# Performance work log

Measured on AMD Instinct MI355X. Metric: run time of the kernel, lower is better.

The kernel has to match this reference:

```python
import jax, jax.numpy as jnp
import numpy as np

N_NODES = 50000
N_EDGES = 1600000
NODE_DIM = 64
EDGE_DIM = 64
HID = 64
EPS = 1e-5


def _linear(x, W, b):
    return x @ W + b


def _layernorm(x, g, b):
    m = jnp.mean(x, axis=-1, keepdims=True)
    v = jnp.mean((x - m) ** 2, axis=-1, keepdims=True)
    return (x - m) * jax.lax.rsqrt(v + EPS) * g + b


def _mlp(x, p, pre):
    # Linear-ReLU, Linear-ReLU, Linear-LayerNorm
    h = jax.nn.relu(_linear(x, p[pre + 'W1'], p[pre + 'b1']))
    h = jax.nn.relu(_linear(h, p[pre + 'W2'], p[pre + 'b2']))
    h = _linear(h, p[pre + 'W3'], p[pre + 'b3'])
    return _layernorm(h, p[pre + 'g'], p[pre + 'beta'])


def setup_inputs() -> dict:
    key = jax.random.key(0)
    ks = jax.random.split(key, 16)
    inp = {
        'node_feat': jax.random.normal(ks[0], (N_NODES, NODE_DIM), jnp.float32),
        'edge_feat': jax.random.normal(ks[1], (N_EDGES, EDGE_DIM), jnp.float32),
        'edge_idx': jax.random.randint(ks[2], (N_EDGES, 2), 0, N_NODES, jnp.int32),
        'node_size': N_NODES,
    }
    s = 0.05
    e_in = EDGE_DIM + 2 * NODE_DIM
    n_in = NODE_DIM + EDGE_DIM
    inp['eW1'] = jax.random.normal(ks[3], (e_in, HID), jnp.float32) * s
    inp['eb1'] = jnp.zeros((HID,), jnp.float32)
    inp['eW2'] = jax.random.normal(ks[4], (HID, HID), jnp.float32) * s
    inp['eb2'] = jnp.zeros((HID,), jnp.float32)
    inp['eW3'] = jax.random.normal(ks[5], (HID, HID), jnp.float32) * s
    inp['eb3'] = jnp.zeros((HID,), jnp.float32)
    inp['eg'] = jnp.ones((HID,), jnp.float32)
    inp['ebeta'] = jnp.zeros((HID,), jnp.float32)
    inp['nW1'] = jax.random.normal(ks[6], (n_in, HID), jnp.float32) * s
    inp['nb1'] = jnp.zeros((HID,), jnp.float32)
    inp['nW2'] = jax.random.normal(ks[7], (HID, HID), jnp.float32) * s
    inp['nb2'] = jnp.zeros((HID,), jnp.float32)
    inp['nW3'] = jax.random.normal(ks[8], (HID, HID), jnp.float32) * s
    inp['nb3'] = jnp.zeros((HID,), jnp.float32)
    inp['ng'] = jnp.ones((HID,), jnp.float32)
    inp['nbeta'] = jnp.zeros((HID,), jnp.float32)
    return inp


def reference(node_feat, edge_feat, edge_idx, node_size,
              eW1, eb1, eW2, eb2, eW3, eb3, eg, ebeta,
              nW1, nb1, nW2, nb2, nW3, nb3, ng, nbeta):
    p = dict(eW1=eW1, eb1=eb1, eW2=eW2, eb2=eb2, eW3=eW3, eb3=eb3, eg=eg, ebeta=ebeta,
             nW1=nW1, nb1=nb1, nW2=nW2, nb2=nb2, nW3=nW3, nb3=nb3, ng=ng, nbeta=nbeta)
    center = edge_idx[:, 0]
    source = edge_idx[:, 1]
    # [E, edge_dim + 2*node_dim]
    stacked = jnp.concatenate([edge_feat, node_feat[center], node_feat[source]], axis=1)
    proc_edge_feat = _mlp(stacked, p, 'e')  # [E, 64]
    # scatter-add aggregate to nodes
    nodal_edge_feat = jax.ops.segment_sum(proc_edge_feat, center, num_segments=node_size)
    stacked_node = jnp.concatenate([node_feat, nodal_edge_feat], axis=1)  # [N, node_dim+64]
    proc_node_feat = _mlp(stacked_node, p, 'n')  # [N, 64]
    return proc_edge_feat, proc_node_feat
```

## Files before the change

kernel.cpp:

```cpp
#include <hip/hip_runtime.h>

typedef unsigned short u16;
typedef unsigned int u32;
typedef __attribute__((ext_vector_type(8))) __bf16 bf16x8;
typedef __attribute__((ext_vector_type(4))) float f32x4;
typedef __attribute__((ext_vector_type(2))) u32 u32x2;
typedef __attribute__((ext_vector_type(4))) u32 u32x4;

__device__ __forceinline__ u16 f2bf(float f) {
    u32 u = __float_as_uint(f);
    u = (u + 0x7FFFu + ((u >> 16) & 1u)) >> 16;
    return (u16)u;
}
__device__ __forceinline__ bf16x8 cvt2bf(f32x4 lo, f32x4 hi) {
    bf16x8 r;
    r[0] = (__bf16)lo[0]; r[1] = (__bf16)lo[1]; r[2] = (__bf16)lo[2]; r[3] = (__bf16)lo[3];
    r[4] = (__bf16)hi[0]; r[5] = (__bf16)hi[1]; r[6] = (__bf16)hi[2]; r[7] = (__bf16)hi[3];
    return r;
}
__device__ __forceinline__ bf16x8 load8f_bf(const float* p) {
    return cvt2bf(*(const f32x4*)p, *(const f32x4*)(p + 4));
}
__device__ __forceinline__ u32 pk2(float x, float y) {
    __bf16 bx = (__bf16)x, by = (__bf16)y;
    return (u32)__builtin_bit_cast(u16, bx) | ((u32)__builtin_bit_cast(u16, by) << 16);
}

#define PK_EW1 0
#define PK_EW2 12288
#define PK_EW3 16384
#define PK_NW1 20480
#define PK_NW2 28672
#define PK_NW3 32768
#define PK_TOTAL 36864

__global__ void pack_weights_kernel(const float* __restrict__ eW1, const float* __restrict__ eW2,
                                    const float* __restrict__ eW3, const float* __restrict__ nW1,
                                    const float* __restrict__ nW2, const float* __restrict__ nW3,
                                    u16* __restrict__ P) {
    int idx = blockIdx.x * blockDim.x + threadIdx.x;
    if (idx >= PK_TOTAL) return;
    const float* W; int base;
    if (idx < PK_EW2)      { W = eW1; base = PK_EW1; }
    else if (idx < PK_EW3) { W = eW2; base = PK_EW2; }
    else if (idx < PK_NW1) { W = eW3; base = PK_EW3; }
    else if (idx < PK_NW2) { W = nW1; base = PK_NW1; }
    else if (idx < PK_NW3) { W = nW2; base = PK_NW2; }
    else                   { W = nW3; base = PK_NW3; }
    int r = idx - base;
    int j = r & 7, lane = (r >> 3) & 63, m = (r >> 9) & 3, s = r >> 11;
    int k = s * 32 + (lane >> 4) * 8 + j;
    int col = 16 * m + (lane & 15);
    P[idx] = f2bf(W[k * 64 + col]);
}

__global__ void degree_kernel(const int* __restrict__ edge_idx, int* __restrict__ deg, int E) {
    int e = blockIdx.x * blockDim.x + threadIdx.x;
    if (e < E) atomicAdd(&deg[edge_idx[2 * e]], 1);
}

__global__ void scan_blocks_kernel(const int* __restrict__ deg, int* __restrict__ off,
                                   int* __restrict__ partials, int N) {
    __shared__ int sh[256];
    const int t = threadIdx.x;
    const int g = blockIdx.x * 256 + t;
    int v = (g < N) ? deg[g] : 0;
    sh[t] = v;
    __syncthreads();
#pragma unroll
    for (int d = 1; d < 256; d <<= 1) {
        int add = (t >= d) ? sh[t - d] : 0;
        __syncthreads();
        sh[t] += add;
        __syncthreads();
    }
    if (g < N) off[g] = sh[t] - v;
    if (t == 255) partials[blockIdx.x] = sh[255];
}

__global__ void scan_partials_kernel(int* __restrict__ partials, int nparts) {
    __shared__ int sh[256];
    const int t = threadIdx.x;
    int v = (t < nparts) ? partials[t] : 0;
    sh[t] = v;
    __syncthreads();
#pragma unroll
    for (int d = 1; d < 256; d <<= 1) {
        int add = (t >= d) ? sh[t - d] : 0;
        __syncthreads();
        sh[t] += add;
        __syncthreads();
    }
    if (t < nparts) partials[t] = sh[t] - v;
}

__global__ void finalize_offsets_kernel(int* __restrict__ off, int* __restrict__ pos,
                                        const int* __restrict__ partials, int N, int E) {
    int g = blockIdx.x * blockDim.x + threadIdx.x;
    if (g < N) {
        int o = off[g] + partials[g >> 8];
        off[g] = o;
        pos[g] = o;
    }
    if (g == 0) off[N] = E;
}

__global__ void fill_csr_kernel(const int* __restrict__ edge_idx, int* __restrict__ pos,
                                int* __restrict__ csr, int E) {
    int e = blockIdx.x * blockDim.x + threadIdx.x;
    if (e < E) {
        int slot = atomicAdd(&pos[edge_idx[2 * e]], 1);
        csr[slot] = e;
    }
}

__global__ __launch_bounds__(256) void gather_csr_kernel(
    const float* __restrict__ proc_edge, const int* __restrict__ off,
    const int* __restrict__ csr, u16* __restrict__ nodal16, int N)
{
    const int wid = threadIdx.x >> 6, lane = threadIdx.x & 63;
    const int n = blockIdx.x * 4 + wid;
    if (n >= N) return;
    const int r = lane >> 4;
    const int q = lane & 15;
    const int beg = off[n], end = off[n + 1];
    f32x4 v0 = 0.0f, v1 = 0.0f, v2 = 0.0f, v3 = 0.0f;
    int j = beg + r;
    for (; j + 12 < end; j += 16) {
        int e0 = csr[j], e1 = csr[j + 4], e2 = csr[j + 8], e3 = csr[j + 12];
        v0 += *(const f32x4*)(proc_edge + (size_t)e0 * 64 + q * 4);
        v1 += *(const f32x4*)(proc_edge + (size_t)e1 * 64 + q * 4);
        v2 += *(const f32x4*)(proc_edge + (size_t)e2 * 64 + q * 4);
        v3 += *(const f32x4*)(proc_edge + (size_t)e3 * 64 + q * 4);
    }
    for (; j < end; j += 4) {
        int e0 = csr[j];
        v0 += *(const f32x4*)(proc_edge + (size_t)e0 * 64 + q * 4);
    }
    v0 += v1; v2 += v3; v0 += v2;
#pragma unroll
    for (int i = 0; i < 4; ++i) {
        v0[i] += __shfl_xor(v0[i], 16, 64);
        v0[i] += __shfl_xor(v0[i], 32, 64);
    }
    if (r == 0) {
        u32x2 pv; pv[0] = pk2(v0[0], v0[1]); pv[1] = pk2(v0[2], v0[3]);
        *(u32x2*)(nodal16 + (size_t)n * 64 + q * 4) = pv;
    }
}

__global__ __launch_bounds__(256) void edge_mlp_kernel(
    const float* __restrict__ node_feat, const float* __restrict__ edge_feat,
    const int* __restrict__ edge_idx, const u16* __restrict__ Pw,
    const float* __restrict__ b1g, const float* __restrict__ b2g, const float* __restrict__ b3g,
    const float* __restrict__ gg, const float* __restrict__ betag,
    float* __restrict__ out_edge, int E)
{
    __shared__ u16 wlds[12288];
    __shared__ u16 stage[4][6144];
    __shared__ float params[5][64];
    const int tid = threadIdx.x;
#pragma unroll
    for (int i = 0; i < 6; ++i) {
        int idx = i * 256 + tid;
        *(u32x4*)(wlds + (size_t)idx * 8) = *(const u32x4*)(Pw + PK_EW1 + (size_t)idx * 8);
    }
    if (tid < 64) {
        params[0][tid] = b1g[tid];
        params[1][tid] = b2g[tid];
        params[2][tid] = b3g[tid];
        params[3][tid] = gg[tid];
        params[4][tid] = betag[tid];
    }
    __syncthreads();

    const int wid = tid >> 6, lane = tid & 63;
    const int er = lane & 15, a = lane >> 4;
    const int e0 = blockIdx.x * 64 + wid * 16 + er;
    const int e = (e0 < E) ? e0 : (E - 1);
    int2 ii = *(const int2*)(edge_idx + 2 * e);
    const int cn = ii.x, sn = ii.y;
    u16* st = stage[wid];
    const int swz = (er & 7) << 4;

#pragma unroll
    for (int s = 0; s < 6; ++s) {
        const float* base;
        if (s < 2)      base = edge_feat + (size_t)e * 64 + s * 32 + a * 8;
        else if (s < 4) base = node_feat + (size_t)cn * 64 + (s - 2) * 32 + a * 8;
        else            base = node_feat + (size_t)sn * 64 + (s - 4) * 32 + a * 8;
        __builtin_amdgcn_global_load_lds(
            (const __attribute__((address_space(1))) void*)base,
            (__attribute__((address_space(3))) void*)(st + (2 * s) * 512), 16, 0, 0);
        __builtin_amdgcn_global_load_lds(
            (const __attribute__((address_space(1))) void*)(base + 4),
            (__attribute__((address_space(3))) void*)(st + (2 * s + 1) * 512), 16, 0, 0);
    }
    __builtin_amdgcn_sched_barrier(0);
    asm volatile("s_waitcnt vmcnt(0)" ::: "memory");
    __builtin_amdgcn_sched_barrier(0);

    f32x4 acc[4];
#pragma unroll
    for (int m = 0; m < 4; ++m) acc[m] = 0.0f;
#pragma unroll
    for (int s = 0; s < 6; ++s) {
        f32x4 lo = *(const f32x4*)((const char*)st + (2 * s) * 1024 + lane * 16);
        f32x4 hi = *(const f32x4*)((const char*)st + (2 * s + 1) * 1024 + lane * 16);
        bf16x8 bf = cvt2bf(lo, hi);
#pragma unroll
        for (int m = 0; m < 4; ++m) {
            bf16x8 af = *(const bf16x8*)(wlds + ((s * 4 + m) * 64 + lane) * 8);
            acc[m] = __builtin_amdgcn_mfma_f32_16x16x32_bf16(af, bf, acc[m], 0, 0, 0);
        }
    }
    __syncthreads();
#pragma unroll
    for (int i = 0; i < 4; ++i) {
        int idx = i * 256 + tid;
        *(u32x4*)(wlds + (size_t)idx * 8) = *(const u32x4*)(Pw + PK_EW2 + (size_t)idx * 8);
    }
    __syncthreads();

    u16* ht = st;
#pragma unroll
    for (int m = 0; m < 4; ++m) {
        float v0 = fmaxf(acc[m][0] + params[0][16 * m + 4 * a + 0], 0.0f);
        float v1 = fmaxf(acc[m][1] + params[0][16 * m + 4 * a + 1], 0.0f);
        float v2 = fmaxf(acc[m][2] + params[0][16 * m + 4 * a + 2], 0.0f);
        float v3 = fmaxf(acc[m][3] + params[0][16 * m + 4 * a + 3], 0.0f);
        u32x2 pv; pv[0] = pk2(v0, v1); pv[1] = pk2(v2, v3);
        int boff = (er * 128 + (16 * m + 4 * a) * 2) ^ swz;
        *(u32x2*)((char*)ht + boff) = pv;
    }
    f32x4 a2[4];
#pragma unroll
    for (int m = 0; m < 4; ++m) a2[m] = 0.0f;
#pragma unroll
    for (int s = 0; s < 2; ++s) {
        int boff = (er * 128 + s * 64 + a * 16) ^ swz;
        bf16x8 bf = *(const bf16x8*)((char*)ht + boff);
#pragma unroll
        for (int m = 0; m < 4; ++m) {
            bf16x8 af = *(const bf16x8*)(wlds + ((s * 4 + m) * 64 + lane) * 8);
            a2[m] = __builtin_amdgcn_mfma_f32_16x16x32_bf16(af, bf, a2[m], 0, 0, 0);
        }
    }
#pragma unroll
    for (int m = 0; m < 4; ++m) {
        float v0 = fmaxf(a2[m][0] + params[1][16 * m + 4 * a + 0], 0.0f);
        float v1 = fmaxf(a2[m][1] + params[1][16 * m + 4 * a + 1], 0.0f);
        float v2 = fmaxf(a2[m][2] + params[1][16 * m + 4 * a + 2], 0.0f);
        float v3 = fmaxf(a2[m][3] + params[1][16 * m + 4 * a + 3], 0.0f);
        u32x2 pv; pv[0] = pk2(v0, v1); pv[1] = pk2(v2, v3);
        int boff = (er * 128 + (16 * m + 4 * a) * 2) ^ swz;
        *(u32x2*)((char*)ht + boff) = pv;
    }
    f32x4 a3[4];
#pragma unroll
    for (int m = 0; m < 4; ++m) a3[m] = 0.0f;
#pragma unroll
    for (int s = 0; s < 2; ++s) {
        int boff = (er * 128 + s * 64 + a * 16) ^ swz;
        bf16x8 bf = *(const bf16x8*)((char*)ht + boff);
#pragma unroll
        for (int m = 0; m < 4; ++m) {
            bf16x8 af = *(const bf16x8*)(wlds + 4096 + ((s * 4 + m) * 64 + lane) * 8);
            a3[m] = __builtin_amdgcn_mfma_f32_16x16x32_bf16(af, bf, a3[m], 0, 0, 0);
        }
    }
    float vals[16], sum = 0.0f, ssq = 0.0f;
#pragma unroll
    for (int m = 0; m < 4; ++m)
#pragma unroll
        for (int r = 0; r < 4; ++r) {
            float v = a3[m][r] + params[2][16 * m + 4 * a + r];
            vals[4 * m + r] = v; sum += v; ssq += v * v;
        }
    sum += __shfl_xor(sum, 16, 64); sum += __shfl_xor(sum, 32, 64);
    ssq += __shfl_xor(ssq, 16, 64); ssq += __shfl_xor(ssq, 32, 64);
    const float mean = sum * 0.015625f;
    const float var = ssq * 0.015625f - mean * mean;
    const float inv = rsqrtf(var + 1e-5f);
    if (e0 < E) {
#pragma unroll
        for (int m = 0; m < 4; ++m) {
            f32x4 o;
#pragma unroll
            for (int r = 0; r < 4; ++r) {
                int f = 16 * m + 4 * a + r;
                o[r] = (vals[4 * m + r] - mean) * inv * params[3][f] + params[4][f];
            }
            *(f32x4*)(out_edge + (size_t)e0 * 64 + 16 * m + 4 * a) = o;
        }
    }
}

__global__ __launch_bounds__(256) void node_mlp_kernel(
    const float* __restrict__ node_feat, const u16* __restrict__ nodal16,
    const u16* __restrict__ Pw,
    const float* __restrict__ b1g, const float* __restrict__ b2g, const float* __restrict__ b3g,
    const float* __restrict__ gg, const float* __restrict__ betag,
    float* __restrict__ out_node, int N)
{
    __shared__ float params[5][64];
    __shared__ u16 htile[4][1024];
    const int tid = threadIdx.x;
    if (tid < 64) {
        params[0][tid] = b1g[tid];
        params[1][tid] = b2g[tid];
        params[2][tid] = b3g[tid];
        params[3][tid] = gg[tid];
        params[4][tid] = betag[tid];
    }
    __syncthreads();
    const int wid = tid >> 6, lane = tid & 63;
    const int er = lane & 15, a = lane >> 4;
    const int nbase = (blockIdx.x * 4 + wid) * 16;
    if (nbase >= N) return;
    const int n = nbase + er;
    u16* ht = htile[wid];
    const int swz = (er & 7) << 4;

    f32x4 acc[4];
#pragma unroll
    for (int m = 0; m < 4; ++m) acc[m] = 0.0f;

#pragma unroll
    for (int s = 0; s < 4; ++s) {
        bf16x8 af[4];
#pragma unroll
        for (int m = 0; m < 4; ++m)
            af[m] = *(const bf16x8*)(Pw + PK_NW1 + ((s * 4 + m) * 64 + lane) * 8);
        bf16x8 bf;
        if (s < 2) bf = load8f_bf(node_feat + (size_t)n * 64 + s * 32 + a * 8);
        else       bf = *(const bf16x8*)(nodal16 + (size_t)n * 64 + (s - 2) * 32 + a * 8);
#pragma unroll
        for (int m = 0; m < 4; ++m)
            acc[m] = __builtin_amdgcn_mfma_f32_16x16x32_bf16(af[m], bf, acc[m], 0, 0, 0);
    }
#pragma unroll
    for (int m = 0; m < 4; ++m) {
        float v0 = fmaxf(acc[m][0] + params[0][16 * m + 4 * a + 0], 0.0f);
        float v1 = fmaxf(acc[m][1] + params[0][16 * m + 4 * a + 1], 0.0f);
        float v2 = fmaxf(acc[m][2] + params[0][16 * m + 4 * a + 2], 0.0f);
        float v3 = fmaxf(acc[m][3] + params[0][16 * m + 4 * a + 3], 0.0f);
        u32x2 pv; pv[0] = pk2(v0, v1); pv[1] = pk2(v2, v3);
        int boff = (er * 128 + (16 * m + 4 * a) * 2) ^ swz;
        *(u32x2*)((char*)ht + boff) = pv;
    }

#pragma unroll
    for (int m = 0; m < 4; ++m) acc[m] = 0.0f;
#pragma unroll
    for (int s = 0; s < 2; ++s) {
        bf16x8 af[4];
#pragma unroll
        for (int m = 0; m < 4; ++m)
            af[m] = *(const bf16x8*)(Pw + PK_NW2 + ((s * 4 + m) * 64 + lane) * 8);
        int boff = (er * 128 + s * 64 + a * 16) ^ swz;
        bf16x8 bf = *(const bf16x8*)((char*)ht + boff);
#pragma unroll
        for (int m = 0; m < 4; ++m)
            acc[m] = __builtin_amdgcn_mfma_f32_16x16x32_bf16(af[m], bf, acc[m], 0, 0, 0);
    }
#pragma unroll
    for (int m = 0; m < 4; ++m) {
        float v0 = fmaxf(acc[m][0] + params[1][16 * m + 4 * a + 0], 0.0f);
        float v1 = fmaxf(acc[m][1] + params[1][16 * m + 4 * a + 1], 0.0f);
        float v2 = fmaxf(acc[m][2] + params[1][16 * m + 4 * a + 2], 0.0f);
        float v3 = fmaxf(acc[m][3] + params[1][16 * m + 4 * a + 3], 0.0f);
        u32x2 pv; pv[0] = pk2(v0, v1); pv[1] = pk2(v2, v3);
        int boff = (er * 128 + (16 * m + 4 * a) * 2) ^ swz;
        *(u32x2*)((char*)ht + boff) = pv;
    }

#pragma unroll
    for (int m = 0; m < 4; ++m) acc[m] = 0.0f;
#pragma unroll
    for (int s = 0; s < 2; ++s) {
        bf16x8 af[4];
#pragma unroll
        for (int m = 0; m < 4; ++m)
            af[m] = *(const bf16x8*)(Pw + PK_NW3 + ((s * 4 + m) * 64 + lane) * 8);
        int boff = (er * 128 + s * 64 + a * 16) ^ swz;
        bf16x8 bf = *(const bf16x8*)((char*)ht + boff);
#pragma unroll
        for (int m = 0; m < 4; ++m)
            acc[m] = __builtin_amdgcn_mfma_f32_16x16x32_bf16(af[m], bf, acc[m], 0, 0, 0);
    }
    float vals[16], sum = 0.0f, ssq = 0.0f;
#pragma unroll
    for (int m = 0; m < 4; ++m)
#pragma unroll
        for (int r = 0; r < 4; ++r) {
            float v = acc[m][r] + params[2][16 * m + 4 * a + r];
            vals[4 * m + r] = v; sum += v; ssq += v * v;
        }
    sum += __shfl_xor(sum, 16, 64); sum += __shfl_xor(sum, 32, 64);
    ssq += __shfl_xor(ssq, 16, 64); ssq += __shfl_xor(ssq, 32, 64);
    const float mean = sum * 0.015625f;
    const float var = ssq * 0.015625f - mean * mean;
    const float inv = rsqrtf(var + 1e-5f);
#pragma unroll
    for (int m = 0; m < 4; ++m) {
        f32x4 o;
#pragma unroll
        for (int r = 0; r < 4; ++r) {
            int f = 16 * m + 4 * a + r;
            o[r] = (vals[4 * m + r] - mean) * inv * params[3][f] + params[4][f];
        }
        *(f32x4*)(out_node + (size_t)n * 64 + 16 * m + 4 * a) = o;
    }
}

extern "C" void kernel_launch(void* const* d_in, const int* in_sizes, int n_in,
                              void* d_out, int out_size, void* d_ws, size_t ws_size,
                              hipStream_t stream) {
    const float* node_feat = (const float*)d_in[0];
    const float* edge_feat = (const float*)d_in[1];
    const int* edge_idx  = (const int*)d_in[2];
    const float* eW1 = (const float*)d_in[4];
    const float* eb1 = (const float*)d_in[5];
    const float* eW2 = (const float*)d_in[6];
    const float* eb2 = (const float*)d_in[7];
    const float* eW3 = (const float*)d_in[8];
    const float* eb3 = (const float*)d_in[9];
    const float* eg  = (const float*)d_in[10];
    const float* ebt = (const float*)d_in[11];
    const float* nW1 = (const float*)d_in[12];
    const float* nb1 = (const float*)d_in[13];
    const float* nW2 = (const float*)d_in[14];
    const float* nb2 = (const float*)d_in[15];
    const float* nW3 = (const float*)d_in[16];
    const float* nb3 = (const float*)d_in[17];
    const float* ng  = (const float*)d_in[18];
    const float* nbt = (const float*)d_in[19];

    const int N = in_sizes[0] / 64;
    const int E = in_sizes[1] / 64;
    const int nparts = (N + 255) / 256;

    char* w = (char*)d_ws;
    int* off      = (int*)w;                    w += (size_t)(N + 1) * 4;
    int* pos      = (int*)w;                    w += (size_t)N * 4;
    int* partials = (int*)w;                    w += 256 * 4;
    int* csr      = (int*)w;                    w += (size_t)E * 4;
    u16* Pw       = (u16*)w;                    w += (size_t)PK_TOTAL * 2;
    w = (char*)(((size_t)w + 255) & ~(size_t)255);
    u16* nodal16  = (u16*)w;

    float* out_edge = (float*)d_out;
    float* out_node = out_edge + (size_t)E * 64;

    pack_weights_kernel<<<(PK_TOTAL + 255) / 256, 256, 0, stream>>>(eW1, eW2, eW3, nW1, nW2, nW3, Pw);

    const int eblocks = (E + 63) / 64;
    edge_mlp_kernel<<<eblocks, 256, 0, stream>>>(node_feat, edge_feat, edge_idx, Pw,
                                                 eb1, eb2, eb3, eg, ebt, out_edge, E);

    hipMemsetAsync(pos, 0, (size_t)N * 4, stream);
    degree_kernel<<<(E + 255) / 256, 256, 0, stream>>>(edge_idx, pos, E);
    scan_blocks_kernel<<<nparts, 256, 0, stream>>>(pos, off, partials, N);
    scan_partials_kernel<<<1, 256, 0, stream>>>(partials, nparts);
    finalize_offsets_kernel<<<(N + 255) / 256, 256, 0, stream>>>(off, pos, partials, N, E);
    fill_csr_kernel<<<(E + 255) / 256, 256, 0, stream>>>(edge_idx, pos, csr, E);

    gather_csr_kernel<<<(N + 3) / 4, 256, 0, stream>>>(out_edge, off, csr, nodal16, N);

    const int nblocks = (N + 63) / 64;
    node_mlp_kernel<<<nblocks, 256, 0, stream>>>(node_feat, nodal16, Pw,
                                                 nb1, nb2, nb3, ng, nbt, out_node, N);
}
```

Baseline: 654.6 us.

## Make edge MLP blocks loop over tiles with double-buffered LDS prefetch

Each edge-MLP block now processes 20 tiles of 64 edges in a loop instead of one. All three edge weight matrices are loaded into LDS once per block, which removes the mid-kernel weight reload and its two barriers. Each iteration issues the async global-to-LDS gather for the next tile, and its edge indices two tiles ahead, before computing the current tile, so memory latency overlaps with the MFMA work. The cost is a much larger LDS footprint (double staging buffers plus all weights), which likely allows only one block per CU. The fixed per-block tile count also leaves a partial last wave of blocks.

```diff
diff --git a/kernel.cpp b/kernel.cpp
--- a/kernel.cpp
+++ b/kernel.cpp
@@ -33,6 +33,8 @@
 #define PK_NW2 28672
 #define PK_NW3 32768
 #define PK_TOTAL 36864
+#define EW_U16 20480
+#define TLOOP 20
 
 __global__ void pack_weights_kernel(const float* __restrict__ eW1, const float* __restrict__ eW2,
                                     const float* __restrict__ eW3, const float* __restrict__ nW1,
@@ -154,16 +156,16 @@
     const int* __restrict__ edge_idx, const u16* __restrict__ Pw,
     const float* __restrict__ b1g, const float* __restrict__ b2g, const float* __restrict__ b3g,
     const float* __restrict__ gg, const float* __restrict__ betag,
-    float* __restrict__ out_edge, int E)
+    float* __restrict__ out_edge, int E, int ntiles)
 {
-    __shared__ u16 wlds[12288];
-    __shared__ u16 stage[4][6144];
+    __shared__ u16 wlds[EW_U16];
+    __shared__ u16 stage[2][4][6144];
     __shared__ float params[5][64];
     const int tid = threadIdx.x;
 #pragma unroll
-    for (int i = 0; i < 6; ++i) {
+    for (int i = 0; i < 10; ++i) {
         int idx = i * 256 + tid;
-        *(u32x4*)(wlds + (size_t)idx * 8) = *(const u32x4*)(Pw + PK_EW1 + (size_t)idx * 8);
+        *(u32x4*)(wlds + (size_t)idx * 8) = *(const u32x4*)(Pw + (size_t)idx * 8);
     }
     if (tid < 64) {
         params[0][tid] = b1g[tid];
@@ -176,123 +178,136 @@
 
     const int wid = tid >> 6, lane = tid & 63;
     const int er = lane & 15, a = lane >> 4;
-    const int e0 = blockIdx.x * 64 + wid * 16 + er;
-    const int e = (e0 < E) ? e0 : (E - 1);
-    int2 ii = *(const int2*)(edge_idx + 2 * e);
-    const int cn = ii.x, sn = ii.y;
-    u16* st = stage[wid];
+    const int tile0 = blockIdx.x * TLOOP;
+    if (tile0 >= ntiles) return;
+    const int eoff = wid * 16 + er;
     const int swz = (er & 7) << 4;
 
-#pragma unroll
-    for (int s = 0; s < 6; ++s) {
-        const float* base;
-        if (s < 2)      base = edge_feat + (size_t)e * 64 + s * 32 + a * 8;
-        else if (s < 4) base = node_feat + (size_t)cn * 64 + (s - 2) * 32 + a * 8;
-        else            base = node_feat + (size_t)sn * 64 + (s - 4) * 32 + a * 8;
-        __builtin_amdgcn_global_load_lds(
-            (const __attribute__((address_space(1))) void*)base,
-            (__attribute__((address_space(3))) void*)(st + (2 * s) * 512), 16, 0, 0);
-        __builtin_amdgcn_global_load_lds(
-            (const __attribute__((address_space(1))) void*)(base + 4),
-            (__attribute__((address_space(3))) void*)(st + (2 * s + 1) * 512), 16, 0, 0);
-    }
-    __builtin_amdgcn_sched_barrier(0);
-    asm volatile("s_waitcnt vmcnt(0)" ::: "memory");
-    __builtin_amdgcn_sched_barrier(0);
-
-    f32x4 acc[4];
-#pragma unroll
-    for (int m = 0; m < 4; ++m) acc[m] = 0.0f;
-#pragma unroll
-    for (int s = 0; s < 6; ++s) {
-        f32x4 lo = *(const f32x4*)((const char*)st + (2 * s) * 1024 + lane * 16);
-        f32x4 hi = *(const f32x4*)((const char*)st + (2 * s + 1) * 1024 + lane * 16);
-        bf16x8 bf = cvt2bf(lo, hi);
+    auto issue_stage = [&](u16* dst, int e_, int cn_, int sn_) {
+#pragma unroll
+        for (int s = 0; s < 6; ++s) {
+            const float* base;
+            if (s < 2)      base = edge_feat + (size_t)e_ * 64 + s * 32 + a * 8;
+            else if (s < 4) base = node_feat + (size_t)cn_ * 64 + (s - 2) * 32 + a * 8;
+            else            base = node_feat + (size_t)sn_ * 64 + (s - 4) * 32 + a * 8;
+            __builtin_amdgcn_global_load_lds(
+                (const __attribute__((address_space(1))) void*)base,
+                (__attribute__((address_space(3))) void*)(dst + (2 * s) * 512), 16, 0, 0);
+            __builtin_amdgcn_global_load_lds(
+                (const __attribute__((address_space(1))) void*)(base + 4),
+                (__attribute__((address_space(3))) void*)(dst + (2 * s + 1) * 512), 16, 0, 0);
+        }
+    };
+    auto clampe = [&](int t) {
+        long long e = (long long)(tile0 + t) * 64 + eoff;
+        return (int)((e < E) ? e : (E - 1));
+    };
+
+    int ec0 = clampe(0);
+    int2 ii0 = *(const int2*)(edge_idx + 2 * ec0);
+    issue_stage(stage[0][wid], ec0, ii0.x, ii0.y);
+    int ecn = clampe(1);
+    int2 iin = *(const int2*)(edge_idx + 2 * ecn);
+
+    for (int t = 0; t < TLOOP; ++t) {
+        u16* cur = stage[t & 1][wid];
+        u16* nxt = stage[(t & 1) ^ 1][wid];
+        issue_stage(nxt, ecn, iin.x, iin.y);
+        int ec2 = clampe(t + 2);
+        int2 ii2 = *(const int2*)(edge_idx + 2 * ec2);
+        __builtin_amdgcn_sched_barrier(0);
+        asm volatile("s_waitcnt vmcnt(13)" ::: "memory");
+        __builtin_amdgcn_sched_barrier(0);
+
+        f32x4 acc[4];
+#pragma unroll
+        for (int m = 0; m < 4; ++m) acc[m] = 0.0f;
+#pragma unroll
+        for (int s = 0; s < 6; ++s) {
+            f32x4 lo = *(const f32x4*)((const char*)cur + (2 * s) * 1024 + lane * 16);
+            f32x4 hi = *(const f32x4*)((const char*)cur + (2 * s + 1) * 1024 + lane * 16);
+            bf16x8 bf = cvt2bf(lo, hi);
+#pragma unroll
+            for (int m = 0; m < 4; ++m) {
+                bf16x8 af = *(const bf16x8*)(wlds + PK_EW1 + ((s * 4 + m) * 64 + lane) * 8);
+                acc[m] = __builtin_amdgcn_mfma_f32_16x16x32_bf16(af, bf, acc[m], 0, 0, 0);
+            }
+        }
+
+        u16* ht = cur;
 #pragma unroll
         for (int m = 0; m < 4; ++m) {
-            bf16x8 af = *(const bf16x8*)(wlds + ((s * 4 + m) * 64 + lane) * 8);
-            acc[m] = __builtin_amdgcn_mfma_f32_16x16x32_bf16(af, bf, acc[m], 0, 0, 0);
-        }
-    }
-    __syncthreads();
-#pragma unroll
-    for (int i = 0; i < 4; ++i) {
-        int idx = i * 256 + tid;
-        *(u32x4*)(wlds + (size_t)idx * 8) = *(const u32x4*)(Pw + PK_EW2 + (size_t)idx * 8);
-    }
-    __syncthreads();
-
-    u16* ht = st;
-#pragma unroll
-    for (int m = 0; m < 4; ++m) {
-        float v0 = fmaxf(acc[m][0] + params[0][16 * m + 4 * a + 0], 0.0f);
-        float v1 = fmaxf(acc[m][1] + params[0][16 * m + 4 * a + 1], 0.0f);
-        float v2 = fmaxf(acc[m][2] + params[0][16 * m + 4 * a + 2], 0.0f);
-        float v3 = fmaxf(acc[m][3] + params[0][16 * m + 4 * a + 3], 0.0f);
-        u32x2 pv; pv[0] = pk2(v0, v1); pv[1] = pk2(v2, v3);
-        int boff = (er * 128 + (16 * m + 4 * a) * 2) ^ swz;
-        *(u32x2*)((char*)ht + boff) = pv;
-    }
-    f32x4 a2[4];
-#pragma unroll
-    for (int m = 0; m < 4; ++m) a2[m] = 0.0f;
-#pragma unroll
-    for (int s = 0; s < 2; ++s) {
-        int boff = (er * 128 + s * 64 + a * 16) ^ swz;
-        bf16x8 bf = *(const bf16x8*)((char*)ht + boff);
+            float v0 = fmaxf(acc[m][0] + params[0][16 * m + 4 * a + 0], 0.0f);
+            float v1 = fmaxf(acc[m][1] + params[0][16 * m + 4 * a + 1], 0.0f);
+            float v2 = fmaxf(acc[m][2] + params[0][16 * m + 4 * a + 2], 0.0f);
+            float v3 = fmaxf(acc[m][3] + params[0][16 * m + 4 * a + 3], 0.0f);
+            u32x2 pv; pv[0] = pk2(v0, v1); pv[1] = pk2(v2, v3);
+            int boff = (er * 128 + (16 * m + 4 * a) * 2) ^ swz;
+            *(u32x2*)((char*)ht + boff) = pv;
+        }
+        f32x4 a2[4];
+#pragma unroll
+        for (int m = 0; m < 4; ++m) a2[m] = 0.0f;
+#pragma unroll
+        for (int s = 0; s < 2; ++s) {
+            int boff = (er * 128 + s * 64 + a * 16) ^ swz;
+            bf16x8 bf = *(const bf16x8*)((char*)ht + boff);
+#pragma unroll
+            for (int m = 0; m < 4; ++m) {
+                bf16x8 af = *(const bf16x8*)(wlds + PK_EW2 + ((s * 4 + m) * 64 + lane) * 8);
+                a2[m] = __builtin_amdgcn_mfma_f32_16x16x32_bf16(af, bf, a2[m], 0, 0, 0);
+            }
+        }
 #pragma unroll
         for (int m = 0; m < 4; ++m) {
-            bf16x8 af = *(const bf16x8*)(wlds + ((s * 4 + m) * 64 + lane) * 8);
-            a2[m] = __builtin_amdgcn_mfma_f32_16x16x32_bf16(af, bf, a2[m], 0, 0, 0);
-        }
-    }
-#pragma unroll
-    for (int m = 0; m < 4; ++m) {
-        float v0 = fmaxf(a2[m][0] + params[1][16 * m + 4 * a + 0], 0.0f);
-        float v1 = fmaxf(a2[m][1] + params[1][16 * m + 4 * a + 1], 0.0f);
-        float v2 = fmaxf(a2[m][2] + params[1][16 * m + 4 * a + 2], 0.0f);
-        float v3 = fmaxf(a2[m][3] + params[1][16 * m + 4 * a + 3], 0.0f);
-        u32x2 pv; pv[0] = pk2(v0, v1); pv[1] = pk2(v2, v3);
-        int boff = (er * 128 + (16 * m + 4 * a) * 2) ^ swz;
-        *(u32x2*)((char*)ht + boff) = pv;
-    }
-    f32x4 a3[4];
-#pragma unroll
-    for (int m = 0; m < 4; ++m) a3[m] = 0.0f;
-#pragma unroll
-    for (int s = 0; s < 2; ++s) {
-        int boff = (er * 128 + s * 64 + a * 16) ^ swz;
-        bf16x8 bf = *(const bf16x8*)((char*)ht + boff);
-#pragma unroll
-        for (int m = 0; m < 4; ++m) {
-            bf16x8 af = *(const bf16x8*)(wlds + 4096 + ((s * 4 + m) * 64 + lane) * 8);
-            a3[m] = __builtin_amdgcn_mfma_f32_16x16x32_bf16(af, bf, a3[m], 0, 0, 0);
-        }
-    }
-    float vals[16], sum = 0.0f, ssq = 0.0f;
-#pragma unroll
-    for (int m = 0; m < 4; ++m)
-#pragma unroll
-        for (int r = 0; r < 4; ++r) {
-            float v = a3[m][r] + params[2][16 * m + 4 * a + r];
-            vals[4 * m + r] = v; sum += v; ssq += v * v;
-        }
-    sum += __shfl_xor(sum, 16, 64); sum += __shfl_xor(sum, 32, 64);
-    ssq += __shfl_xor(ssq, 16, 64); ssq += __shfl_xor(ssq, 32, 64);
-    const float mean = sum * 0.015625f;
-    const float var = ssq * 0.015625f - mean * mean;
-    const float inv = rsqrtf(var + 1e-5f);
-    if (e0 < E) {
-#pragma unroll
-        for (int m = 0; m < 4; ++m) {
-            f32x4 o;
+            float v0 = fmaxf(a2[m][0] + params[1][16 * m + 4 * a + 0], 0.0f);
+            float v1 = fmaxf(a2[m][1] + params[1][16 * m + 4 * a + 1], 0.0f);
+            float v2 = fmaxf(a2[m][2] + params[1][16 * m + 4 * a + 2], 0.0f);
+            float v3 = fmaxf(a2[m][3] + params[1][16 * m + 4 * a + 3], 0.0f);
+            u32x2 pv; pv[0] = pk2(v0, v1); pv[1] = pk2(v2, v3);
+            int boff = (er * 128 + (16 * m + 4 * a) * 2) ^ swz;
+            *(u32x2*)((char*)ht + boff) = pv;
+        }
+        f32x4 a3[4];
+#pragma unroll
+        for (int m = 0; m < 4; ++m) a3[m] = 0.0f;
+#pragma unroll
+        for (int s = 0; s < 2; ++s) {
+            int boff = (er * 128 + s * 64 + a * 16) ^ swz;
+            bf16x8 bf = *(const bf16x8*)((char*)ht + boff);
+#pragma unroll
+            for (int m = 0; m < 4; ++m) {
+                bf16x8 af = *(const bf16x8*)(wlds + PK_EW3 + ((s * 4 + m) * 64 + lane) * 8);
+                a3[m] = __builtin_amdgcn_mfma_f32_16x16x32_bf16(af, bf, a3[m], 0, 0, 0);
+            }
+        }
+        float vals[16], sum = 0.0f, ssq = 0.0f;
+#pragma unroll
+        for (int m = 0; m < 4; ++m)
 #pragma unroll
             for (int r = 0; r < 4; ++r) {
-                int f = 16 * m + 4 * a + r;
-                o[r] = (vals[4 * m + r] - mean) * inv * params[3][f] + params[4][f];
+                float v = a3[m][r] + params[2][16 * m + 4 * a + r];
+                vals[4 * m + r] = v; sum += v; ssq += v * v;
             }
-            *(f32x4*)(out_edge + (size_t)e0 * 64 + 16 * m + 4 * a) = o;
-        }
+        sum += __shfl_xor(sum, 16, 64); sum += __shfl_xor(sum, 32, 64);
+        ssq += __shfl_xor(ssq, 16, 64); ssq += __shfl_xor(ssq, 32, 64);
+        const float mean = sum * 0.015625f;
+        const float var = ssq * 0.015625f - mean * mean;
+        const float inv = rsqrtf(var + 1e-5f);
+        const long long eg = (long long)(tile0 + t) * 64 + eoff;
+        if (eg < E) {
+#pragma unroll
+            for (int m = 0; m < 4; ++m) {
+                f32x4 o;
+#pragma unroll
+                for (int r = 0; r < 4; ++r) {
+                    int f = 16 * m + 4 * a + r;
+                    o[r] = (vals[4 * m + r] - mean) * inv * params[3][f] + params[4][f];
+                }
+                *(f32x4*)(out_edge + (size_t)eg * 64 + 16 * m + 4 * a) = o;
+            }
+        }
+        ecn = ec2; iin = ii2;
     }
 }
 
@@ -455,9 +470,10 @@
 
     pack_weights_kernel<<<(PK_TOTAL + 255) / 256, 256, 0, stream>>>(eW1, eW2, eW3, nW1, nW2, nW3, Pw);
 
-    const int eblocks = (E + 63) / 64;
+    const int ntiles = (E + 63) / 64;
+    const int eblocks = (ntiles + TLOOP - 1) / TLOOP;
     edge_mlp_kernel<<<eblocks, 256, 0, stream>>>(node_feat, edge_feat, edge_idx, Pw,
-                                                 eb1, eb2, eb3, eg, ebt, out_edge, E);
+                                                 eb1, eb2, eb3, eg, ebt, out_edge, E, ntiles);
 
     hipMemsetAsync(pos, 0, (size_t)N * 4, stream);
     degree_kernel<<<(E + 255) / 256, 256, 0, stream>>>(edge_idx, pos, E);
```

Measured after the change: 637.5 us. 1.03x faster.
